# Performance work log

Measured on AMD Instinct MI355X. Metric: run time of the kernel, lower is better.

Reference implementation:

```python
import jax, jax.numpy as jnp
import numpy as np

N = 100000
E = 1600000
IN_C, HID_C, OUT_C = 64, 64, 32


def setup_inputs() -> dict:
    key = jax.random.key(0)
    ks = jax.random.split(key, 8)
    x = jax.random.normal(ks[0], (N, IN_C), dtype=jnp.float32)
    edge_index = jax.random.randint(ks[1], (2, E), 0, N, dtype=jnp.int64)
    # GCNConv weights (glorot-ish scale) and biases
    W1 = jax.random.normal(ks[2], (IN_C, HID_C), dtype=jnp.float32) / np.sqrt(IN_C)
    b1 = jnp.zeros((HID_C,), dtype=jnp.float32)
    W2 = jax.random.normal(ks[3], (HID_C, HID_C), dtype=jnp.float32) / np.sqrt(HID_C)
    b2 = jnp.zeros((HID_C,), dtype=jnp.float32)
    Wlin = jax.random.normal(ks[4], (HID_C, OUT_C), dtype=jnp.float32) / np.sqrt(HID_C)
    blin = jnp.zeros((OUT_C,), dtype=jnp.float32)
    return {"x": x, "edge_index": edge_index, "W1": W1, "b1": b1,
            "W2": W2, "b2": b2, "Wlin": Wlin, "blin": blin}


def _gcn_norm(edge_index):
    # PyG GCNConv default: add self-loops, symmetric normalization.
    loop = jnp.arange(N, dtype=edge_index.dtype)
    row = jnp.concatenate([edge_index[0], loop])  # source nodes [E+N]
    col = jnp.concatenate([edge_index[1], loop])  # target nodes [E+N]
    deg = jax.ops.segment_sum(jnp.ones_like(col, dtype=jnp.float32), col,
                              num_segments=N)
    dinv = jnp.where(deg > 0, deg ** -0.5, 0.0)
    norm = dinv[row] * dinv[col]  # [E+N]
    return row, col, norm


def _gcn_conv(h, W, b, row, col, norm):
    h = h @ W                                  # [N, F_out]
    msg = h[row] * norm[:, None]               # gather + scale, [E+N, F_out]
    out = jax.ops.segment_sum(msg, col, num_segments=N)  # scatter-add
    return out + b


def reference(x, edge_index, W1, b1, W2, b2, Wlin, blin):
    row, col, norm = _gcn_norm(edge_index)
    h = jax.nn.relu(_gcn_conv(x, W1, b1, row, col, norm))
    h = jax.nn.relu(_gcn_conv(h, W2, b2, row, col, norm))
    return h @ Wlin + blin
```

## Files before the change

kernel.cpp:

```cpp
#include <hip/hip_runtime.h>
#include <hip/hip_fp16.h>

#define IN_C 64
#define HID_C 64
#define OUT_C 32
#define S_NODES  512
#define S_CAP  12288
#define CHUNK_E 2048

typedef _Float16 f16_t;
typedef f16_t f16x2 __attribute__((ext_vector_type(2)));

__device__ __forceinline__ float dot2(unsigned int a, unsigned int b, float c) {
#if __has_builtin(__builtin_amdgcn_fdot2)
    return __builtin_amdgcn_fdot2(*(f16x2*)&a, *(f16x2*)&b, c, false);
#else
    float2 af = __half22float2(*(__half2*)&a);
    float2 bf = __half22float2(*(__half2*)&b);
    return fmaf(af.x, bf.x, fmaf(af.y, bf.y, c));
#endif
}

__global__ void prep(const int* ei32, int* flag, int n_check,
                     const float* __restrict__ W1, const float* __restrict__ W2,
                     const float* __restrict__ Wlin,
                     unsigned short* __restrict__ Wh1,
                     unsigned short* __restrict__ Wh2,
                     unsigned short* __restrict__ Whl) {
    __shared__ int s_any;
    if (threadIdx.x == 0) s_any = 0;
    __syncthreads();
    int any = 0;
    for (int i = threadIdx.x; i < n_check; i += blockDim.x) {
        if (ei32[2 * i + 1] != 0) any = 1;
    }
    if (any) atomicOr(&s_any, 1);
    for (int i = threadIdx.x; i < 4096; i += 256) {
        int r = i >> 6, c = i & 63;
        f16_t h1 = (f16_t)W1[r * 64 + c];
        f16_t h2 = (f16_t)W2[r * 64 + c];
        Wh1[c * 64 + r] = *(unsigned short*)&h1;
        Wh2[c * 64 + r] = *(unsigned short*)&h2;
    }
    for (int i = threadIdx.x; i < 2048; i += 256) {
        int r = i >> 5, c = i & 31;
        f16_t h = (f16_t)Wlin[r * 32 + c];
        Whl[c * 64 + r] = *(unsigned short*)&h;
    }
    __syncthreads();
    if (threadIdx.x == 0) *flag = (s_any == 0) ? 1 : 0;
}

__device__ __forceinline__ int ld_edge(const void* ei, int idx, int is64) {
    if (is64) return (int)((const long long*)ei)[idx];
    return ((const int*)ei)[idx];
}

__global__ __launch_bounds__(256) void bin_edges(const void* ei, int E, const int* flag,
                                                 int* bcur, int NB,
                                                 int* __restrict__ staging) {
    __shared__ int cnt[256], boff[256], lcur[256], gbase[256];
    __shared__ int stg[CHUNK_E];
    __shared__ int s_is64;
    int tid = threadIdx.x;
    if (tid == 0) s_is64 = *flag;
    cnt[tid] = 0;
    __syncthreads();
    int is64 = s_is64;
    int e0 = blockIdx.x * CHUNK_E;
    int e1 = min(E, e0 + CHUNK_E);
    for (int e = e0 + tid; e < e1; e += 256) {
        int dst = ld_edge(ei, E + e, is64);
        atomicAdd(&cnt[dst >> 9], 1);
    }
    __syncthreads();
    int v = cnt[tid];
    gbase[tid] = v;
    __syncthreads();
    for (int o = 1; o < 256; o <<= 1) {
        int u = (tid >= o) ? gbase[tid - o] : 0;
        __syncthreads();
        gbase[tid] += u;
        __syncthreads();
    }
    boff[tid] = gbase[tid] - v;
    lcur[tid] = boff[tid];
    __syncthreads();
    for (int e = e0 + tid; e < e1; e += 256) {
        int src = ld_edge(ei, e, is64);
        int dst = ld_edge(ei, E + e, is64);
        int p = atomicAdd(&lcur[dst >> 9], 1);
        stg[p] = src | ((dst & 511) << 17);
    }
    __syncthreads();
    if (tid < NB && cnt[tid] > 0) gbase[tid] = atomicAdd(&bcur[tid], cnt[tid]);
    __syncthreads();
    int sw = tid >> 4, sl = tid & 15;
    for (int b = sw; b < NB; b += 16) {
        int c = cnt[b];
        if (c == 0) continue;
        int o = boff[b], g = gbase[b];
        size_t gb = (size_t)b * S_CAP;
        for (int j = sl; j < c; j += 16) {
            if (g + j < S_CAP) staging[gb + g + j] = stg[o + j];
        }
    }
}

__global__ __launch_bounds__(256) void place_fine(const int* __restrict__ staging,
                                                  const int* __restrict__ bcur,
                                                  int* __restrict__ offs,
                                                  float* __restrict__ dinv,
                                                  int* __restrict__ rec, int N, int NB) {
    __shared__ int sdeg[S_NODES];
    __shared__ int tsum[256];
    __shared__ int curs[S_NODES];
    __shared__ int sb[256];
    int tid = threadIdx.x;
    int vcnt = (tid < NB) ? min(bcur[tid], S_CAP) : 0;
    sb[tid] = vcnt;
    sdeg[tid] = 0;
    sdeg[tid + 256] = 0;
    __syncthreads();
    for (int o = 1; o < 256; o <<= 1) {
        int u = (tid >= o) ? sb[tid - o] : 0;
        __syncthreads();
        sb[tid] += u;
        __syncthreads();
    }
    int cnt = min(bcur[blockIdx.x], S_CAP);
    int bbase = sb[blockIdx.x] - cnt;
    if (blockIdx.x == NB - 1 && tid == 0) offs[N] = sb[255];
    int base = blockIdx.x * S_NODES;
    int nn = min(S_NODES, N - base);
    size_t sbase = (size_t)blockIdx.x * S_CAP;
    for (int j = tid; j < cnt; j += 256) atomicAdd(&sdeg[staging[sbase + j] >> 17], 1);
    __syncthreads();
    int d0 = sdeg[2 * tid], d1 = sdeg[2 * tid + 1];
    tsum[tid] = d0 + d1;
    __syncthreads();
    for (int o = 1; o < 256; o <<= 1) {
        int v = (tid >= o) ? tsum[tid - o] : 0;
        __syncthreads();
        tsum[tid] += v;
        __syncthreads();
    }
    int pre = bbase + ((tid == 0) ? 0 : tsum[tid - 1]);
    curs[2 * tid] = pre;
    curs[2 * tid + 1] = pre + d0;
    if (2 * tid < nn) {
        offs[base + 2 * tid] = pre;
        dinv[base + 2 * tid] = rsqrtf((float)(d0 + 1));
    }
    if (2 * tid + 1 < nn) {
        offs[base + 2 * tid + 1] = pre + d0;
        dinv[base + 2 * tid + 1] = rsqrtf((float)(d1 + 1));
    }
    __syncthreads();
    for (int j = tid; j < cnt; j += 256) {
        int pk = staging[sbase + j];
        int p = atomicAdd(&curs[pk >> 17], 1);
        rec[p] = pk & 0x1FFFF;
    }
}

__global__ __launch_bounds__(256) void gemm64(const float* __restrict__ in,
                                              const unsigned short* __restrict__ Wh,
                                              unsigned short* __restrict__ out,
                                              const float* __restrict__ dinv, int n) {
    __shared__ uint4 sA[32 * 8];
    int tid = threadIdx.x;
    int lane = tid & 63, wave = tid >> 6;
    unsigned int wu[32];
    {
        const uint4* col = (const uint4*)(Wh + (size_t)lane * 64);
#pragma unroll
        for (int j = 0; j < 8; j++) {
            uint4 w4 = col[j];
            wu[4 * j] = w4.x; wu[4 * j + 1] = w4.y;
            wu[4 * j + 2] = w4.z; wu[4 * j + 3] = w4.w;
        }
    }
    int base = blockIdx.x * 32;
    const float2* A2 = (const float2*)in;
    int lim = n * 32;
    for (int i = tid; i < 1024; i += 256) {
        int gi = base * 32 + i;
        float2 v = (gi < lim) ? A2[gi] : make_float2(0.f, 0.f);
        ((__half2*)sA)[i] = __floats2half2_rn(v.x, v.y);
    }
    __syncthreads();
    int r0 = base + wave * 8;
    int r1 = min(r0 + 8, n);
    for (int r = r0; r < r1; r++) {
        int rr = r - base;
        float a0 = 0.f, a1 = 0.f;
#pragma unroll
        for (int j = 0; j < 8; j++) {
            uint4 u = sA[rr * 8 + j];
            a0 = dot2(u.x, wu[4 * j], a0);
            a1 = dot2(u.y, wu[4 * j + 1], a1);
            a0 = dot2(u.z, wu[4 * j + 2], a0);
            a1 = dot2(u.w, wu[4 * j + 3], a1);
        }
        __half hv = __float2half_rn((a0 + a1) * dinv[r]);
        out[(size_t)r * 64 + lane] = *(unsigned short*)&hv;
    }
}

template <int MODE>
__global__ __launch_bounds__(256) void agg_gemm(const unsigned short* __restrict__ t,
                                                const int* __restrict__ offs,
                                                const int* __restrict__ rec,
                                                const float* __restrict__ dinv,
                                                const float* __restrict__ bias,
                                                const unsigned short* __restrict__ Wh,
                                                unsigned short* __restrict__ outh,
                                                float* __restrict__ outf,
                                                const float* __restrict__ blin, int n) {
    constexpr int COLS = (MODE == 0) ? 64 : 32;
    __shared__ unsigned short sW[64 * COLS];
    __shared__ uint4 srow[4][8];
    int tid = threadIdx.x;
    int lane = tid & 63, wave = tid >> 6;
    {
        const uint4* s4 = (const uint4*)Wh;
        uint4* d4 = (uint4*)sW;
        for (int i = tid; i < 64 * COLS / 8; i += 256) d4[i] = s4[i];
    }
    __syncthreads();
    int c = (MODE == 0) ? lane : (lane & 31);
    unsigned int wu[32];
    {
        const uint4* col = ((const uint4*)sW) + c * 8;
#pragma unroll
        for (int j = 0; j < 8; j++) {
            uint4 w4 = col[j];
            wu[4 * j] = w4.x; wu[4 * j + 1] = w4.y;
            wu[4 * j + 2] = w4.z; wu[4 * j + 3] = w4.w;
        }
    }
    int g = lane >> 3;
    int gl = lane & 7;
    const float4* b4 = (const float4*)bias;
    float4 bb0 = b4[gl * 2], bb1 = b4[gl * 2 + 1];
    float bl = (MODE == 1) ? blin[c] : 0.f;
    const uint4* t4 = (const uint4*)t;
    int nw = gridDim.x * 4;
    for (int node = blockIdx.x * 4 + wave; node < n; node += nw) {
        int beg = offs[node], end = offs[node + 1];
        int m = end - beg + 1;
        float s[8] = {0.f, 0.f, 0.f, 0.f, 0.f, 0.f, 0.f, 0.f};
        for (int i = 0; i < m; i += 32) {
            int srcs[4];
            float ws[4];
#pragma unroll
            for (int u = 0; u < 4; u++) {
                int it = i + u * 8 + g;
                srcs[u] = (it == 0) ? node : ((it < m) ? rec[beg + it - 1] : node);
                ws[u] = (it < m) ? 1.f : 0.f;
            }
            uint4 vs[4];
#pragma unroll
            for (int u = 0; u < 4; u++) vs[u] = t4[(size_t)srcs[u] * 8 + gl];
#pragma unroll
            for (int u = 0; u < 4; u++) {
                float w = ws[u];
                float2 f0 = __half22float2(*(__half2*)&vs[u].x);
                float2 f1 = __half22float2(*(__half2*)&vs[u].y);
                float2 f2 = __half22float2(*(__half2*)&vs[u].z);
                float2 f3 = __half22float2(*(__half2*)&vs[u].w);
                s[0] = fmaf(f0.x, w, s[0]);
                s[1] = fmaf(f0.y, w, s[1]);
                s[2] = fmaf(f1.x, w, s[2]);
                s[3] = fmaf(f1.y, w, s[3]);
                s[4] = fmaf(f2.x, w, s[4]);
                s[5] = fmaf(f2.y, w, s[5]);
                s[6] = fmaf(f3.x, w, s[6]);
                s[7] = fmaf(f3.y, w, s[7]);
            }
        }
#pragma unroll
        for (int k = 0; k < 8; k++) {
            s[k] += __shfl_xor(s[k], 8);
            s[k] += __shfl_xor(s[k], 16);
            s[k] += __shfl_xor(s[k], 32);
        }
        float d = dinv[node];
        if (g == 0) {
            float o0 = fmaxf(fmaf(s[0], d, bb0.x), 0.f);
            float o1 = fmaxf(fmaf(s[1], d, bb0.y), 0.f);
            float o2 = fmaxf(fmaf(s[2], d, bb0.z), 0.f);
            float o3 = fmaxf(fmaf(s[3], d, bb0.w), 0.f);
            float o4 = fmaxf(fmaf(s[4], d, bb1.x), 0.f);
            float o5 = fmaxf(fmaf(s[5], d, bb1.y), 0.f);
            float o6 = fmaxf(fmaf(s[6], d, bb1.z), 0.f);
            float o7 = fmaxf(fmaf(s[7], d, bb1.w), 0.f);
            __half2 p0 = __floats2half2_rn(o0, o1);
            __half2 p1 = __floats2half2_rn(o2, o3);
            __half2 p2 = __floats2half2_rn(o4, o5);
            __half2 p3 = __floats2half2_rn(o6, o7);
            srow[wave][gl] = make_uint4(*(unsigned int*)&p0, *(unsigned int*)&p1,
                                        *(unsigned int*)&p2, *(unsigned int*)&p3);
        }
        float a0 = 0.f, a1 = 0.f;
#pragma unroll
        for (int j = 0; j < 8; j++) {
            uint4 u = srow[wave][j];
            a0 = dot2(u.x, wu[4 * j], a0);
            a1 = dot2(u.y, wu[4 * j + 1], a1);
            a0 = dot2(u.z, wu[4 * j + 2], a0);
            a1 = dot2(u.w, wu[4 * j + 3], a1);
        }
        float val = a0 + a1;
        if (MODE == 0) {
            __half hv = __float2half_rn(val * d);
            outh[(size_t)node * 64 + lane] = *(unsigned short*)&hv;
        } else {
            if (lane < 32) outf[(size_t)node * 32 + c] = bl + val;
        }
    }
}

extern "C" void kernel_launch(void* const* d_in, const int* in_sizes, int n_in,
                              void* d_out, int out_size, void* d_ws, size_t ws_size,
                              hipStream_t stream) {
    (void)n_in; (void)out_size; (void)ws_size;
    const float* x    = (const float*)d_in[0];
    const void*  ei   = d_in[1];
    const float* W1   = (const float*)d_in[2];
    const float* b1   = (const float*)d_in[3];
    const float* W2   = (const float*)d_in[4];
    const float* b2   = (const float*)d_in[5];
    const float* Wlin = (const float*)d_in[6];
    const float* blin = (const float*)d_in[7];
    float* out = (float*)d_out;

    const int N = in_sizes[0] / IN_C;
    const int E = in_sizes[1] / 2;
    const int NB = (N + S_NODES - 1) / S_NODES;
    const int NEB = (E + CHUNK_E - 1) / CHUNK_E;

    char* ws = (char*)d_ws;
    size_t off = 0;
    auto alloc = [&](size_t bytes) -> void* {
        size_t a = (off + 255) & ~(size_t)255;
        off = a + bytes;
        return (void*)(ws + a);
    };
    int*   flag    = (int*)  alloc(4);
    int*   offs    = (int*)  alloc((size_t)(N + 1) * 4);
    float* dinv    = (float*)alloc((size_t)N * 4);
    int*   bcur    = (int*)  alloc((size_t)NB * 4);
    int*   rec     = (int*)  alloc((size_t)E * 4);
    int*   staging = (int*)  alloc((size_t)NB * S_CAP * 4);
    unsigned short* tbuf = (unsigned short*)alloc((size_t)N * HID_C * 2);
    unsigned short* acc  = (unsigned short*)alloc((size_t)N * HID_C * 2);
    unsigned short* Wh1  = (unsigned short*)alloc(64 * 64 * 2);
    unsigned short* Wh2  = (unsigned short*)alloc(64 * 64 * 2);
    unsigned short* Whl  = (unsigned short*)alloc(64 * 32 * 2);

    hipMemsetAsync(bcur, 0, (size_t)NB * 4, stream);

    int n_check = E < 4096 ? E : 4096;
    prep<<<1, 256, 0, stream>>>((const int*)ei, flag, n_check, W1, W2, Wlin,
                                Wh1, Wh2, Whl);
    bin_edges<<<NEB, 256, 0, stream>>>(ei, E, flag, bcur, NB, staging);
    place_fine<<<NB, 256, 0, stream>>>(staging, bcur, offs, dinv, rec, N, NB);

    const int GB = (N + 31) / 32;
    gemm64<<<GB, 256, 0, stream>>>(x, Wh1, tbuf, dinv, N);

    int AG = 2048;
    if (AG * 4 > N) AG = (N + 3) / 4;
    agg_gemm<0><<<AG, 256, 0, stream>>>(tbuf, offs, rec, dinv, b1, Wh2,
                                        acc, nullptr, nullptr, N);
    agg_gemm<1><<<AG, 256, 0, stream>>>(acc, offs, rec, dinv, b2, Whl,
                                        nullptr, out, blin, N);
}
```

Baseline: 289.0 us.

## Assign contiguous node runs per wave and split full/tail edge loops

The aggregation kernels now give each wave four consecutive nodes instead of a grid-stride loop, and reuse the previous node's end offset as the next begin. The gather loop is split into a full-chunk path that needs no bounds checks or weight multiplies, plus a predicated tail. Shared-memory weights are padded to a stride of nine uint4 to avoid bank conflicts when each lane reads its own column. The launch grid now scales with N, so more blocks are launched and each one reloads the weights once.

```diff
diff --git a/kernel.cpp b/kernel.cpp
--- a/kernel.cpp
+++ b/kernel.cpp
@@ -219,26 +219,22 @@
                                                 float* __restrict__ outf,
                                                 const float* __restrict__ blin, int n) {
     constexpr int COLS = (MODE == 0) ? 64 : 32;
-    __shared__ unsigned short sW[64 * COLS];
+    __shared__ uint4 sW[COLS][9];
     __shared__ uint4 srow[4][8];
     int tid = threadIdx.x;
     int lane = tid & 63, wave = tid >> 6;
     {
         const uint4* s4 = (const uint4*)Wh;
-        uint4* d4 = (uint4*)sW;
-        for (int i = tid; i < 64 * COLS / 8; i += 256) d4[i] = s4[i];
+        for (int i = tid; i < COLS * 8; i += 256) sW[i >> 3][i & 7] = s4[i];
     }
     __syncthreads();
     int c = (MODE == 0) ? lane : (lane & 31);
     unsigned int wu[32];
-    {
-        const uint4* col = ((const uint4*)sW) + c * 8;
-#pragma unroll
-        for (int j = 0; j < 8; j++) {
-            uint4 w4 = col[j];
-            wu[4 * j] = w4.x; wu[4 * j + 1] = w4.y;
-            wu[4 * j + 2] = w4.z; wu[4 * j + 3] = w4.w;
-        }
+#pragma unroll
+    for (int j = 0; j < 8; j++) {
+        uint4 w4 = sW[c][j];
+        wu[4 * j] = w4.x; wu[4 * j + 1] = w4.y;
+        wu[4 * j + 2] = w4.z; wu[4 * j + 3] = w4.w;
     }
     int g = lane >> 3;
     int gl = lane & 7;
@@ -246,47 +242,73 @@
     float4 bb0 = b4[gl * 2], bb1 = b4[gl * 2 + 1];
     float bl = (MODE == 1) ? blin[c] : 0.f;
     const uint4* t4 = (const uint4*)t;
-    int nw = gridDim.x * 4;
-    for (int node = blockIdx.x * 4 + wave; node < n; node += nw) {
-        int beg = offs[node], end = offs[node + 1];
+    int node0 = (blockIdx.x * 4 + wave) * 4;
+    if (node0 >= n) return;
+    int beg = offs[node0];
+    for (int k = 0; k < 4; k++) {
+        int node = node0 + k;
+        if (node >= n) break;
+        int end = offs[node + 1];
+        float d = dinv[node];
         int m = end - beg + 1;
         float s[8] = {0.f, 0.f, 0.f, 0.f, 0.f, 0.f, 0.f, 0.f};
-        for (int i = 0; i < m; i += 32) {
-            int srcs[4];
-            float ws[4];
+        int i = 0;
+        for (; m - i >= 32; i += 32) {
+            uint4 vs[4];
 #pragma unroll
             for (int u = 0; u < 4; u++) {
                 int it = i + u * 8 + g;
-                srcs[u] = (it == 0) ? node : ((it < m) ? rec[beg + it - 1] : node);
-                ws[u] = (it < m) ? 1.f : 0.f;
+                int src = (it == 0) ? node : rec[beg + it - 1];
+                vs[u] = t4[(size_t)src * 8 + gl];
             }
-            uint4 vs[4];
-#pragma unroll
-            for (int u = 0; u < 4; u++) vs[u] = t4[(size_t)srcs[u] * 8 + gl];
 #pragma unroll
             for (int u = 0; u < 4; u++) {
-                float w = ws[u];
                 float2 f0 = __half22float2(*(__half2*)&vs[u].x);
                 float2 f1 = __half22float2(*(__half2*)&vs[u].y);
                 float2 f2 = __half22float2(*(__half2*)&vs[u].z);
                 float2 f3 = __half22float2(*(__half2*)&vs[u].w);
-                s[0] = fmaf(f0.x, w, s[0]);
-                s[1] = fmaf(f0.y, w, s[1]);
-                s[2] = fmaf(f1.x, w, s[2]);
-                s[3] = fmaf(f1.y, w, s[3]);
-                s[4] = fmaf(f2.x, w, s[4]);
-                s[5] = fmaf(f2.y, w, s[5]);
-                s[6] = fmaf(f3.x, w, s[6]);
-                s[7] = fmaf(f3.y, w, s[7]);
+                s[0] += f0.x; s[1] += f0.y; s[2] += f1.x; s[3] += f1.y;
+                s[4] += f2.x; s[5] += f2.y; s[6] += f3.x; s[7] += f3.y;
             }
         }
-#pragma unroll
-        for (int k = 0; k < 8; k++) {
-            s[k] += __shfl_xor(s[k], 8);
-            s[k] += __shfl_xor(s[k], 16);
-            s[k] += __shfl_xor(s[k], 32);
-        }
-        float d = dinv[node];
+        int nit = m - i;
+        if (nit > 0) {
+            uint4 vs[4];
+            float ws[4];
+#pragma unroll
+            for (int u = 0; u < 4; u++) {
+                if (u * 8 < nit) {
+                    int it = i + u * 8 + g;
+                    int src = (it == 0) ? node : ((it < m) ? rec[beg + it - 1] : node);
+                    ws[u] = (it < m) ? 1.f : 0.f;
+                    vs[u] = t4[(size_t)src * 8 + gl];
+                }
+            }
+#pragma unroll
+            for (int u = 0; u < 4; u++) {
+                if (u * 8 < nit) {
+                    float w = ws[u];
+                    float2 f0 = __half22float2(*(__half2*)&vs[u].x);
+                    float2 f1 = __half22float2(*(__half2*)&vs[u].y);
+                    float2 f2 = __half22float2(*(__half2*)&vs[u].z);
+                    float2 f3 = __half22float2(*(__half2*)&vs[u].w);
+                    s[0] = fmaf(f0.x, w, s[0]);
+                    s[1] = fmaf(f0.y, w, s[1]);
+                    s[2] = fmaf(f1.x, w, s[2]);
+                    s[3] = fmaf(f1.y, w, s[3]);
+                    s[4] = fmaf(f2.x, w, s[4]);
+                    s[5] = fmaf(f2.y, w, s[5]);
+                    s[6] = fmaf(f3.x, w, s[6]);
+                    s[7] = fmaf(f3.y, w, s[7]);
+                }
+            }
+        }
+#pragma unroll
+        for (int kk = 0; kk < 8; kk++) {
+            s[kk] += __shfl_xor(s[kk], 8);
+            s[kk] += __shfl_xor(s[kk], 16);
+            s[kk] += __shfl_xor(s[kk], 32);
+        }
         if (g == 0) {
             float o0 = fmaxf(fmaf(s[0], d, bb0.x), 0.f);
             float o1 = fmaxf(fmaf(s[1], d, bb0.y), 0.f);
@@ -319,6 +341,7 @@
         } else {
             if (lane < 32) outf[(size_t)node * 32 + c] = bl + val;
         }
+        beg = end;
     }
 }
 
@@ -371,10 +394,9 @@
     const int GB = (N + 31) / 32;
     gemm64<<<GB, 256, 0, stream>>>(x, Wh1, tbuf, dinv, N);
 
-    int AG = 2048;
-    if (AG * 4 > N) AG = (N + 3) / 4;
-    agg_gemm<0><<<AG, 256, 0, stream>>>(tbuf, offs, rec, dinv, b1, Wh2,
-                                        acc, nullptr, nullptr, N);
-    agg_gemm<1><<<AG, 256, 0, stream>>>(acc, offs, rec, dinv, b2, Whl,
-                                        nullptr, out, blin, N);
-}
+    const int AGB = (N + 15) / 16;
+    agg_gemm<0><<<AGB, 256, 0, stream>>>(tbuf, offs, rec, dinv, b1, Wh2,
+                                         acc, nullptr, nullptr, N);
+    agg_gemm<1><<<AGB, 256, 0, stream>>>(acc, offs, rec, dinv, b2, Whl,
+                                         nullptr, out, blin, N);
+}
```

New measurement: 307.5 us. 6.4% more time.

## Split fused aggregate+GEMM kernels into separate aggregate and GEMM launches

Applied to the files above, without the earlier changes.

Replaces the two persistent fused aggregate-then-transform kernels with separate kernels: a one-wave-per-node aggregate kernel that writes fp16 activations, a templated gemm64 that now takes fp16 input, and a new gemm32 for the final linear layer. The intent is simpler per-kernel code and better occupancy, with no per-node LDS round trip or weight-register pressure in the gather loop. In exchange it adds two extra launches and extra global-memory round trips of the N×64 fp16 activations.

```diff
diff --git a/kernel.cpp b/kernel.cpp
--- a/kernel.cpp
+++ b/kernel.cpp
@@ -164,7 +164,8 @@
     }
 }
 
-__global__ __launch_bounds__(256) void gemm64(const float* __restrict__ in,
+template <int IN_F32>
+__global__ __launch_bounds__(256) void gemm64(const void* __restrict__ in,
                                               const unsigned short* __restrict__ Wh,
                                               unsigned short* __restrict__ out,
                                               const float* __restrict__ dinv, int n) {
@@ -182,12 +183,21 @@
         }
     }
     int base = blockIdx.x * 32;
-    const float2* A2 = (const float2*)in;
-    int lim = n * 32;
-    for (int i = tid; i < 1024; i += 256) {
-        int gi = base * 32 + i;
-        float2 v = (gi < lim) ? A2[gi] : make_float2(0.f, 0.f);
-        ((__half2*)sA)[i] = __floats2half2_rn(v.x, v.y);
+    if (IN_F32) {
+        const float2* A2 = (const float2*)in;
+        int lim = n * 32;
+        for (int i = tid; i < 1024; i += 256) {
+            int gi = base * 32 + i;
+            float2 v = (gi < lim) ? A2[gi] : make_float2(0.f, 0.f);
+            ((__half2*)sA)[i] = __floats2half2_rn(v.x, v.y);
+        }
+    } else {
+        const uint2* A2 = (const uint2*)in;
+        int lim = n * 16;
+        for (int i = tid; i < 512; i += 256) {
+            int gi = base * 16 + i;
+            ((uint2*)sA)[i] = (gi < lim) ? A2[gi] : make_uint2(0u, 0u);
+        }
     }
     __syncthreads();
     int r0 = base + wave * 8;
@@ -208,31 +218,87 @@
     }
 }
 
-template <int MODE>
-__global__ __launch_bounds__(256) void agg_gemm(const unsigned short* __restrict__ t,
-                                                const int* __restrict__ offs,
-                                                const int* __restrict__ rec,
-                                                const float* __restrict__ dinv,
-                                                const float* __restrict__ bias,
-                                                const unsigned short* __restrict__ Wh,
-                                                unsigned short* __restrict__ outh,
-                                                float* __restrict__ outf,
-                                                const float* __restrict__ blin, int n) {
-    constexpr int COLS = (MODE == 0) ? 64 : 32;
-    __shared__ unsigned short sW[64 * COLS];
-    __shared__ uint4 srow[4][8];
+__global__ void aggregate(const unsigned short* __restrict__ t,
+                          const int* __restrict__ offs, const int* __restrict__ rec,
+                          const float* __restrict__ dinv, const float* __restrict__ bias,
+                          unsigned short* __restrict__ acc, int n) {
+    int wave = (blockIdx.x * blockDim.x + threadIdx.x) >> 6;
+    int lane = threadIdx.x & 63;
+    if (wave >= n) return;
+    int g = lane >> 3;
+    int gl = lane & 7;
+    int beg = offs[wave], end = offs[wave + 1];
+    int m = end - beg + 1;
+    const uint4* t4 = (const uint4*)t;
+    float s[8] = {0.f, 0.f, 0.f, 0.f, 0.f, 0.f, 0.f, 0.f};
+    for (int i = 0; i < m; i += 32) {
+        int srcs[4];
+        float ws[4];
+#pragma unroll
+        for (int u = 0; u < 4; u++) {
+            int it = i + u * 8 + g;
+            srcs[u] = (it == 0) ? wave : ((it < m) ? rec[beg + it - 1] : wave);
+            ws[u] = (it < m) ? 1.f : 0.f;
+        }
+        uint4 vs[4];
+#pragma unroll
+        for (int u = 0; u < 4; u++) vs[u] = t4[(size_t)srcs[u] * 8 + gl];
+#pragma unroll
+        for (int u = 0; u < 4; u++) {
+            float w = ws[u];
+            float2 f0 = __half22float2(*(__half2*)&vs[u].x);
+            float2 f1 = __half22float2(*(__half2*)&vs[u].y);
+            float2 f2 = __half22float2(*(__half2*)&vs[u].z);
+            float2 f3 = __half22float2(*(__half2*)&vs[u].w);
+            s[0] = fmaf(f0.x, w, s[0]);
+            s[1] = fmaf(f0.y, w, s[1]);
+            s[2] = fmaf(f1.x, w, s[2]);
+            s[3] = fmaf(f1.y, w, s[3]);
+            s[4] = fmaf(f2.x, w, s[4]);
+            s[5] = fmaf(f2.y, w, s[5]);
+            s[6] = fmaf(f3.x, w, s[6]);
+            s[7] = fmaf(f3.y, w, s[7]);
+        }
+    }
+#pragma unroll
+    for (int k = 0; k < 8; k++) {
+        s[k] += __shfl_xor(s[k], 8);
+        s[k] += __shfl_xor(s[k], 16);
+        s[k] += __shfl_xor(s[k], 32);
+    }
+    if (g == 0) {
+        float d = dinv[wave];
+        const float4* b4 = (const float4*)bias;
+        float4 bb0 = b4[gl * 2], bb1 = b4[gl * 2 + 1];
+        float o0 = fmaxf(fmaf(s[0], d, bb0.x), 0.f);
+        float o1 = fmaxf(fmaf(s[1], d, bb0.y), 0.f);
+        float o2 = fmaxf(fmaf(s[2], d, bb0.z), 0.f);
+        float o3 = fmaxf(fmaf(s[3], d, bb0.w), 0.f);
+        float o4 = fmaxf(fmaf(s[4], d, bb1.x), 0.f);
+        float o5 = fmaxf(fmaf(s[5], d, bb1.y), 0.f);
+        float o6 = fmaxf(fmaf(s[6], d, bb1.z), 0.f);
+        float o7 = fmaxf(fmaf(s[7], d, bb1.w), 0.f);
+        __half2 p0 = __floats2half2_rn(o0, o1);
+        __half2 p1 = __floats2half2_rn(o2, o3);
+        __half2 p2 = __floats2half2_rn(o4, o5);
+        __half2 p3 = __floats2half2_rn(o6, o7);
+        ((uint4*)acc)[(size_t)wave * 8 + gl] =
+            make_uint4(*(unsigned int*)&p0, *(unsigned int*)&p1,
+                       *(unsigned int*)&p2, *(unsigned int*)&p3);
+    }
+}
+
+__global__ __launch_bounds__(256) void gemm32(const unsigned short* __restrict__ in,
+                                              const unsigned short* __restrict__ Wh,
+                                              const float* __restrict__ b,
+                                              float* __restrict__ out, int n) {
+    __shared__ uint4 sA[32 * 8];
     int tid = threadIdx.x;
     int lane = tid & 63, wave = tid >> 6;
-    {
-        const uint4* s4 = (const uint4*)Wh;
-        uint4* d4 = (uint4*)sW;
-        for (int i = tid; i < 64 * COLS / 8; i += 256) d4[i] = s4[i];
-    }
-    __syncthreads();
-    int c = (MODE == 0) ? lane : (lane & 31);
+    int c = lane & 31;
     unsigned int wu[32];
     {
-        const uint4* col = ((const uint4*)sW) + c * 8;
+        const uint4* col = (const uint4*)(Wh + (size_t)c * 64);
 #pragma unroll
         for (int j = 0; j < 8; j++) {
             uint4 w4 = col[j];
@@ -240,85 +306,29 @@
             wu[4 * j + 2] = w4.z; wu[4 * j + 3] = w4.w;
         }
     }
-    int g = lane >> 3;
-    int gl = lane & 7;
-    const float4* b4 = (const float4*)bias;
-    float4 bb0 = b4[gl * 2], bb1 = b4[gl * 2 + 1];
-    float bl = (MODE == 1) ? blin[c] : 0.f;
-    const uint4* t4 = (const uint4*)t;
-    int nw = gridDim.x * 4;
-    for (int node = blockIdx.x * 4 + wave; node < n; node += nw) {
-        int beg = offs[node], end = offs[node + 1];
-        int m = end - beg + 1;
-        float s[8] = {0.f, 0.f, 0.f, 0.f, 0.f, 0.f, 0.f, 0.f};
-        for (int i = 0; i < m; i += 32) {
-            int srcs[4];
-            float ws[4];
-#pragma unroll
-            for (int u = 0; u < 4; u++) {
-                int it = i + u * 8 + g;
-                srcs[u] = (it == 0) ? node : ((it < m) ? rec[beg + it - 1] : node);
-                ws[u] = (it < m) ? 1.f : 0.f;
-            }
-            uint4 vs[4];
-#pragma unroll
-            for (int u = 0; u < 4; u++) vs[u] = t4[(size_t)srcs[u] * 8 + gl];
-#pragma unroll
-            for (int u = 0; u < 4; u++) {
-                float w = ws[u];
-                float2 f0 = __half22float2(*(__half2*)&vs[u].x);
-                float2 f1 = __half22float2(*(__half2*)&vs[u].y);
-                float2 f2 = __half22float2(*(__half2*)&vs[u].z);
-                float2 f3 = __half22float2(*(__half2*)&vs[u].w);
-                s[0] = fmaf(f0.x, w, s[0]);
-                s[1] = fmaf(f0.y, w, s[1]);
-                s[2] = fmaf(f1.x, w, s[2]);
-                s[3] = fmaf(f1.y, w, s[3]);
-                s[4] = fmaf(f2.x, w, s[4]);
-                s[5] = fmaf(f2.y, w, s[5]);
-                s[6] = fmaf(f3.x, w, s[6]);
-                s[7] = fmaf(f3.y, w, s[7]);
-            }
-        }
-#pragma unroll
-        for (int k = 0; k < 8; k++) {
-            s[k] += __shfl_xor(s[k], 8);
-            s[k] += __shfl_xor(s[k], 16);
-            s[k] += __shfl_xor(s[k], 32);
-        }
-        float d = dinv[node];
-        if (g == 0) {
-            float o0 = fmaxf(fmaf(s[0], d, bb0.x), 0.f);
-            float o1 = fmaxf(fmaf(s[1], d, bb0.y), 0.f);
-            float o2 = fmaxf(fmaf(s[2], d, bb0.z), 0.f);
-            float o3 = fmaxf(fmaf(s[3], d, bb0.w), 0.f);
-            float o4 = fmaxf(fmaf(s[4], d, bb1.x), 0.f);
-            float o5 = fmaxf(fmaf(s[5], d, bb1.y), 0.f);
-            float o6 = fmaxf(fmaf(s[6], d, bb1.z), 0.f);
-            float o7 = fmaxf(fmaf(s[7], d, bb1.w), 0.f);
-            __half2 p0 = __floats2half2_rn(o0, o1);
-            __half2 p1 = __floats2half2_rn(o2, o3);
-            __half2 p2 = __floats2half2_rn(o4, o5);
-            __half2 p3 = __floats2half2_rn(o6, o7);
-            srow[wave][gl] = make_uint4(*(unsigned int*)&p0, *(unsigned int*)&p1,
-                                        *(unsigned int*)&p2, *(unsigned int*)&p3);
-        }
+    float bl = b[c];
+    int base = blockIdx.x * 32;
+    const uint2* A2 = (const uint2*)in;
+    int lim = n * 16;
+    for (int i = tid; i < 512; i += 256) {
+        int gi = base * 16 + i;
+        ((uint2*)sA)[i] = (gi < lim) ? A2[gi] : make_uint2(0u, 0u);
+    }
+    __syncthreads();
+    int r0 = base + wave * 8;
+    int r1 = min(r0 + 8, n);
+    for (int r = r0; r < r1; r++) {
+        int rr = r - base;
         float a0 = 0.f, a1 = 0.f;
 #pragma unroll
         for (int j = 0; j < 8; j++) {
-            uint4 u = srow[wave][j];
+            uint4 u = sA[rr * 8 + j];
             a0 = dot2(u.x, wu[4 * j], a0);
             a1 = dot2(u.y, wu[4 * j + 1], a1);
             a0 = dot2(u.z, wu[4 * j + 2], a0);
             a1 = dot2(u.w, wu[4 * j + 3], a1);
         }
-        float val = a0 + a1;
-        if (MODE == 0) {
-            __half hv = __float2half_rn(val * d);
-            outh[(size_t)node * 64 + lane] = *(unsigned short*)&hv;
-        } else {
-            if (lane < 32) outf[(size_t)node * 32 + c] = bl + val;
-        }
+        if (lane < 32) out[(size_t)r * 32 + c] = bl + a0 + a1;
     }
 }
 
@@ -369,12 +379,9 @@
     place_fine<<<NB, 256, 0, stream>>>(staging, bcur, offs, dinv, rec, N, NB);
 
     const int GB = (N + 31) / 32;
-    gemm64<<<GB, 256, 0, stream>>>(x, Wh1, tbuf, dinv, N);
-
-    int AG = 2048;
-    if (AG * 4 > N) AG = (N + 3) / 4;
-    agg_gemm<0><<<AG, 256, 0, stream>>>(tbuf, offs, rec, dinv, b1, Wh2,
-                                        acc, nullptr, nullptr, N);
-    agg_gemm<1><<<AG, 256, 0, stream>>>(acc, offs, rec, dinv, b2, Whl,
-                                        nullptr, out, blin, N);
-}
+    gemm64<1><<<GB, 256, 0, stream>>>(x, Wh1, tbuf, dinv, N);
+    aggregate<<<(N + 3) / 4, 256, 0, stream>>>(tbuf, offs, rec, dinv, b1, acc, N);
+    gemm64<0><<<GB, 256, 0, stream>>>(acc, Wh2, tbuf, dinv, N);
+    aggregate<<<(N + 3) / 4, 256, 0, stream>>>(tbuf, offs, rec, dinv, b2, acc, N);
+    gemm32<<<GB, 256, 0, stream>>>(acc, Whl, blin, out, N);
+}
```

New measurement: 287.5 us. About the same (-0.5%).
